# Optimization experiments

Measured on AMD Instinct MI355X. Metric: run time of the kernel, lower is better.

## Reference

```python
import jax, jax.numpy as jnp
import numpy as np

N = 50000       # nodes
E = 1600000     # edges
G = 16          # graphs in batch
NUMCHIP = 16    # node features
NUMEDGE = 8     # edge features
H = 32          # hidden_channels
NEG = 0.2       # LeakyReLU slope (PyG GAT default)


def _wegat_conv(x, ea, src, dst, Wn, bn, We, be, att):
    """Edge-weighted GAT conv: returns (node_out [N,H], edge_out [E,NUMEDGE])."""
    xn = x @ Wn + bn                      # [N, H]
    ea2 = ea @ We + be                    # [E, NUMEDGE]
    xi = xn[dst]                          # [E, H] target features
    xj = xn[src]                          # [E, H] source features
    logits = jnp.concatenate([xi, xj, ea2], axis=-1) @ att   # [E]
    logits = jax.nn.leaky_relu(logits, NEG)
    # numerically stable softmax over incoming edges per destination node
    m = jax.ops.segment_max(logits, dst, num_segments=N)
    m = jnp.where(jnp.isfinite(m), m, 0.0)
    p = jnp.exp(logits - m[dst])
    s = jax.ops.segment_sum(p, dst, num_segments=N)
    alpha = p / (s[dst] + 1e-16)          # [E]
    out = jax.ops.segment_sum(xj * alpha[:, None], dst, num_segments=N)  # [N, H]
    return out, ea2


def setup_inputs() -> dict:
    key = jax.random.key(0)
    ks = jax.random.split(key, 24)

    def gl(k, shape):
        fan_in = shape[0] if len(shape) > 1 else shape[0]
        return jax.random.normal(k, shape, dtype=jnp.float32) * (1.0 / np.sqrt(fan_in))

    inp = {
        'x': jax.random.normal(ks[0], (N, NUMCHIP), dtype=jnp.float32),
        'edge_attr': jax.random.normal(ks[1], (E, NUMEDGE), dtype=jnp.float32),
        'edge_index': jax.random.randint(ks[2], (2, E), 0, N, dtype=jnp.int64),
        'batch': jnp.sort(jax.random.randint(ks[3], (N,), 0, G, dtype=jnp.int64)),
        # layer 1
        'Wn1': gl(ks[4], (NUMCHIP, H)), 'bn1': jnp.zeros((H,), jnp.float32),
        'We1': gl(ks[5], (NUMEDGE, NUMEDGE)), 'be1': jnp.zeros((NUMEDGE,), jnp.float32),
        'att1': gl(ks[6], (2 * H + NUMEDGE,)),
        # layer 2
        'Wn2': gl(ks[7], (H, H)), 'bn2': jnp.zeros((H,), jnp.float32),
        'We2': gl(ks[8], (NUMEDGE, NUMEDGE)), 'be2': jnp.zeros((NUMEDGE,), jnp.float32),
        'att2': gl(ks[9], (2 * H + NUMEDGE,)),
        # layer 3
        'Wn3': gl(ks[10], (H, H)), 'bn3': jnp.zeros((H,), jnp.float32),
        'We3': gl(ks[11], (NUMEDGE, NUMEDGE)), 'be3': jnp.zeros((NUMEDGE,), jnp.float32),
        'att3': gl(ks[12], (2 * H + NUMEDGE,)),
        # head
        'Wlin': gl(ks[13], (H, 1)), 'blin': jnp.zeros((1,), jnp.float32),
    }
    return inp


def reference(x, edge_attr, edge_index, batch,
              Wn1, bn1, We1, be1, att1,
              Wn2, bn2, We2, be2, att2,
              Wn3, bn3, We3, be3, att3,
              Wlin, blin):
    src, dst = edge_index[0], edge_index[1]
    x1, ea1 = _wegat_conv(x, edge_attr, src, dst, Wn1, bn1, We1, be1, att1)
    x1 = jax.nn.relu(x1)  # NOTE: original's edge_attr.relu() is a discarded no-op
    x2, ea2 = _wegat_conv(x1, ea1, src, dst, Wn2, bn2, We2, be2, att2)
    x2 = jax.nn.relu(x2)
    x3, _ = _wegat_conv(x2, ea2, src, dst, Wn3, bn3, We3, be3, att3)
    # global mean pool over graphs
    sums = jax.ops.segment_sum(x3, batch, num_segments=G)                   # [G, H]
    cnts = jax.ops.segment_sum(jnp.ones((N,), x3.dtype), batch, num_segments=G)
    pooled = sums / jnp.maximum(cnts, 1.0)[:, None]
    return pooled @ Wlin + blin  # [G, 1]
```

## Files before the change

### kernel.cpp

```cpp
#include <hip/hip_runtime.h>
#include <math.h>
#include <limits.h>


__global__ __launch_bounds__(256) void hist_kernel(const int* __restrict__ dst, int* cnt, int E) {
    int e = blockIdx.x * blockDim.x + threadIdx.x;
    if (e < E) atomicAdd(&cnt[dst[e]], 1);
}

__global__ __launch_bounds__(1024) void scan_kernel(const int* __restrict__ cnt,
                                                    int* rowptr, int* cursor, int n) {
    __shared__ int sums[1024];
    int t = threadIdx.x;
    int CH = (n + 1023) >> 10;
    int s0 = t * CH;
    int s1 = min(n, s0 + CH);
    int local = 0;
    for (int i = s0; i < s1; i++) local += cnt[i];
    sums[t] = local;
    __syncthreads();
    for (int off = 1; off < 1024; off <<= 1) {
        int v = (t >= off) ? sums[t - off] : 0;
        __syncthreads();
        sums[t] += v;
        __syncthreads();
    }
    int run = (t == 0) ? 0 : sums[t - 1];
    for (int i = s0; i < s1; i++) {
        rowptr[i] = run;
        cursor[i] = run;
        run += cnt[i];
    }
    if (t == 1023) rowptr[n] = sums[1023];
}

__global__ __launch_bounds__(256) void scatter_kernel(const int* __restrict__ src,
                                                      const int* __restrict__ dst,
                                                      int* cursor, int2* __restrict__ pack, int E) {
    int e = blockIdx.x * blockDim.x + threadIdx.x;
    if (e >= E) return;
    int d = dst[e];
    int pos = atomicAdd(&cursor[d], 1);
    pack[pos] = make_int2(src[e], e);
}

template <int IN>
__global__ __launch_bounds__(256) void node_linear(const float* __restrict__ xin,
                                                   const float* __restrict__ Wn,
                                                   const float* __restrict__ bn,
                                                   const float* __restrict__ att,
                                                   float* __restrict__ xn,
                                                   float* __restrict__ ai,
                                                   float* __restrict__ aj, int n) {
    int t = blockIdx.x * blockDim.x + threadIdx.x;
    int node = t >> 5;
    int h = t & 31;
    if (node >= n) return;
    float xv[IN];
    const float4* xr = (const float4*)(xin + (size_t)node * IN);
#pragma unroll
    for (int q = 0; q < IN / 4; q++) {
        float4 f = xr[q];
        xv[4 * q + 0] = f.x;
        xv[4 * q + 1] = f.y;
        xv[4 * q + 2] = f.z;
        xv[4 * q + 3] = f.w;
    }
    float acc = bn[h];
#pragma unroll
    for (int k = 0; k < IN; k++) {
        acc = fmaf(xv[k], Wn[k * 32 + h], acc);
    }
    xn[node * 32 + h] = acc;
    float pi = acc * att[h];
    float pj = acc * att[32 + h];
#pragma unroll
    for (int off = 16; off > 0; off >>= 1) {
        pi += __shfl_xor(pi, off);
        pj += __shfl_xor(pj, off);
    }
    if (h == 0) {
        ai[node] = pi;
        aj[node] = pj;
    }
}

__global__ __launch_bounds__(256) void edge_chain(
    const float* __restrict__ ein,
    const float* __restrict__ We1, const float* __restrict__ be1, const float* __restrict__ a1,
    const float* __restrict__ We2, const float* __restrict__ be2, const float* __restrict__ a2,
    const float* __restrict__ We3, const float* __restrict__ be3, const float* __restrict__ a3,
    float4* __restrict__ aet, int E) {
    int e = blockIdx.x * blockDim.x + threadIdx.x;
    if (e >= E) return;
    const float4* p = (const float4*)(ein + (size_t)e * 8);
    float4 x0 = p[0], x1 = p[1];
    float v[8] = {x0.x, x0.y, x0.z, x0.w, x1.x, x1.y, x1.z, x1.w};
    float t[8], u[8];
    float d1 = 0.f, d2 = 0.f, d3 = 0.f;
#pragma unroll
    for (int j = 0; j < 8; j++) {
        float a = be1[j];
#pragma unroll
        for (int k = 0; k < 8; k++) a = fmaf(v[k], We1[k * 8 + j], a);
        t[j] = a;
        d1 = fmaf(a, a1[j], d1);
    }
#pragma unroll
    for (int j = 0; j < 8; j++) {
        float a = be2[j];
#pragma unroll
        for (int k = 0; k < 8; k++) a = fmaf(t[k], We2[k * 8 + j], a);
        u[j] = a;
        d2 = fmaf(a, a2[j], d2);
    }
#pragma unroll
    for (int j = 0; j < 8; j++) {
        float a = be3[j];
#pragma unroll
        for (int k = 0; k < 8; k++) a = fmaf(u[k], We3[k * 8 + j], a);
        d3 = fmaf(a, a3[j], d3);
    }
    aet[e] = make_float4(d1, d2, d3, 0.f);
}

__global__ __launch_bounds__(256) void row_sort(const int2* __restrict__ pack,
                                                const int* __restrict__ rowptr,
                                                const float4* __restrict__ aet,
                                                int* __restrict__ srcs,
                                                float* __restrict__ aes1,
                                                float* __restrict__ aes2,
                                                float* __restrict__ aes3, int n) {
    int wave = (blockIdx.x * blockDim.x + threadIdx.x) >> 6;
    int lane = threadIdx.x & 63;
    if (wave >= n) return;
    int row = rowptr[wave];
    int deg = rowptr[wave + 1] - row;
    if (deg == 0) return;

    if (deg <= 64) {
        int e = INT_MAX, s = 0;
        if (lane < deg) {
            int2 q = pack[row + lane];
            s = q.x;
            e = q.y;
        }
#pragma unroll
        for (int size = 2; size <= 64; size <<= 1) {
#pragma unroll
            for (int stride = size >> 1; stride > 0; stride >>= 1) {
                int pe = __shfl_xor(e, stride);
                int ps = __shfl_xor(s, stride);
                bool up = ((lane & size) == 0);
                bool lower = ((lane & stride) == 0);
                bool keep = (lower == up) ? (e <= pe) : (e >= pe);
                e = keep ? e : pe;
                s = keep ? s : ps;
            }
        }
        if (lane < deg) {
            srcs[row + lane] = s;
            float4 a = aet[e];
            aes1[row + lane] = a.x;
            aes2[row + lane] = a.y;
            aes3[row + lane] = a.z;
        }
        return;
    }

    int prev = -1;
    for (int r = 0; r < deg; r++) {
        int mn = INT_MAX, ms = 0;
        for (int k = lane; k < deg; k += 64) {
            int2 q = pack[row + k];
            if (q.y > prev && q.y < mn) {
                mn = q.y;
                ms = q.x;
            }
        }
#pragma unroll
        for (int off = 32; off > 0; off >>= 1) {
            int oe = __shfl_xor(mn, off);
            int os = __shfl_xor(ms, off);
            if (oe < mn) {
                mn = oe;
                ms = os;
            }
        }
        if (lane == 0) {
            srcs[row + r] = ms;
            float4 a = aet[mn];
            aes1[row + r] = a.x;
            aes2[row + r] = a.y;
            aes3[row + r] = a.z;
        }
        prev = mn;
    }
}

__global__ __launch_bounds__(256) void gat_aggregate(const float* __restrict__ xn,
                                                     const float* __restrict__ ai,
                                                     const float* __restrict__ aj,
                                                     const float* __restrict__ aes,
                                                     const int* __restrict__ rowptr,
                                                     const int* __restrict__ srcs,
                                                     float* __restrict__ xout,
                                                     int n, int relu_out) {
    int wave = (blockIdx.x * blockDim.x + threadIdx.x) >> 6;
    int lane = threadIdx.x & 63;
    if (wave >= n) return;
    int node = wave;
    int row = rowptr[node];
    int deg = rowptr[node + 1] - row;
    int h = lane & 31;
    if (deg == 0) {
        if (lane < 32) xout[node * 32 + h] = 0.f;
        return;
    }
    float a_i = ai[node];
    const int* sp = srcs + row;
    const float* ap = aes + row;

    if (deg <= 64) {
        int s = 0;
        float lg = -INFINITY;
        bool act = (lane < deg);
        if (act) {
            s = sp[lane];
            lg = a_i + aj[s] + ap[lane];
            lg = (lg >= 0.f) ? lg : 0.2f * lg;
        }
        float mx = lg;
#pragma unroll
        for (int off = 32; off > 0; off >>= 1) mx = fmaxf(mx, __shfl_xor(mx, off));
        float p = act ? expf(lg - mx) : 0.f;
        float ps = 0.f;
        for (int j = 0; j < deg; j++) ps += __shfl(p, j);
        float al = p / (ps + 1e-16f);
        float acc = 0.f;
        int j = 0;
        for (; j + 3 < deg; j += 4) {
            float a0 = __shfl(al, j);
            int s0 = __shfl(s, j);
            float a1 = __shfl(al, j + 1);
            int s1 = __shfl(s, j + 1);
            float a2 = __shfl(al, j + 2);
            int s2 = __shfl(s, j + 2);
            float a3 = __shfl(al, j + 3);
            int s3 = __shfl(s, j + 3);
            float g0 = xn[s0 * 32 + h];
            float g1 = xn[s1 * 32 + h];
            float g2 = xn[s2 * 32 + h];
            float g3 = xn[s3 * 32 + h];
            acc = __fadd_rn(acc, __fmul_rn(a0, g0));
            acc = __fadd_rn(acc, __fmul_rn(a1, g1));
            acc = __fadd_rn(acc, __fmul_rn(a2, g2));
            acc = __fadd_rn(acc, __fmul_rn(a3, g3));
        }
        for (; j < deg; j++) {
            float aj_ = __shfl(al, j);
            int sj = __shfl(s, j);
            acc = __fadd_rn(acc, __fmul_rn(aj_, xn[sj * 32 + h]));
        }
        float o = acc;
        if (relu_out) o = fmaxf(o, 0.f);
        if (lane < 32) xout[node * 32 + h] = o;
        return;
    }

    float mx = -INFINITY;
    for (int k = lane; k < deg; k += 64) {
        float lg = a_i + aj[sp[k]] + ap[k];
        lg = (lg >= 0.f) ? lg : 0.2f * lg;
        mx = fmaxf(mx, lg);
    }
#pragma unroll
    for (int off = 32; off > 0; off >>= 1) mx = fmaxf(mx, __shfl_xor(mx, off));

    float ps = 0.f;
    for (int base = 0; base < deg; base += 64) {
        int k = base + lane;
        float p = 0.f;
        if (k < deg) {
            float lg = a_i + aj[sp[k]] + ap[k];
            lg = (lg >= 0.f) ? lg : 0.2f * lg;
            p = expf(lg - mx);
        }
        int csize = min(64, deg - base);
        for (int j = 0; j < csize; j++) ps += __shfl(p, j);
    }
    float denom = ps + 1e-16f;
    float acc = 0.f;
    for (int base = 0; base < deg; base += 64) {
        int k = base + lane;
        float p = 0.f;
        int s = 0;
        if (k < deg) {
            s = sp[k];
            float lg = a_i + aj[s] + ap[k];
            lg = (lg >= 0.f) ? lg : 0.2f * lg;
            p = expf(lg - mx);
        }
        float al = p / denom;
        int csize = min(64, deg - base);
        for (int j = 0; j < csize; j++) {
            float aj_ = __shfl(al, j);
            int sj = __shfl(s, j);
            acc = __fadd_rn(acc, __fmul_rn(aj_, xn[sj * 32 + h]));
        }
    }
    float o = acc;
    if (relu_out) o = fmaxf(o, 0.f);
    if (lane < 32) xout[node * 32 + h] = o;
}

__global__ __launch_bounds__(1024) void poolhead_kernel(const float* __restrict__ x3,
                                                        const int* __restrict__ batch,
                                                        const float* __restrict__ Wlin,
                                                        const float* __restrict__ blin,
                                                        float* out, int n) {
    __shared__ float red[32][33];
    int g = blockIdx.x;
    int t = threadIdx.x;
    int h = t & 31;
    int rowl = t >> 5;
    int lo = 0, hi = n;
    while (lo < hi) {
        int m = (lo + hi) >> 1;
        if (batch[m] < g) lo = m + 1; else hi = m;
    }
    int start = lo;
    lo = start; hi = n;
    while (lo < hi) {
        int m = (lo + hi) >> 1;
        if (batch[m] < g + 1) lo = m + 1; else hi = m;
    }
    int end = lo;
    float acc = 0.f;
    for (int i = start + rowl; i < end; i += 32) acc += x3[i * 32 + h];
    red[rowl][h] = acc;
    __syncthreads();
    if (rowl < 16) red[rowl][h] = red[rowl][h] + red[rowl + 16][h];
    __syncthreads();
    if (rowl < 8) red[rowl][h] = red[rowl][h] + red[rowl + 8][h];
    __syncthreads();
    if (rowl < 4) red[rowl][h] = red[rowl][h] + red[rowl + 4][h];
    __syncthreads();
    if (rowl < 2) red[rowl][h] = red[rowl][h] + red[rowl + 2][h];
    __syncthreads();
    if (rowl == 0) {
        float s = red[0][h] + red[1][h];
        float c = fmaxf((float)(end - start), 1.f);
        float pooled = s / c;
        float sum = 0.f;
        for (int k = 0; k < 32; k++) {
            float v = __shfl(pooled, k, 32);
            sum = __fadd_rn(sum, __fmul_rn(v, Wlin[k]));
        }
        if (h == 0) out[g] = sum + blin[0];
    }
}

extern "C" void kernel_launch(void* const* d_in, const int* in_sizes, int n_in,
                              void* d_out, int out_size, void* d_ws, size_t ws_size,
                              hipStream_t stream) {
    const float* x    = (const float*)d_in[0];
    const float* ea0  = (const float*)d_in[1];
    const int* ei     = (const int*)d_in[2];
    const int* batch  = (const int*)d_in[3];
    const float* Wn[3] = {(const float*)d_in[4], (const float*)d_in[9],  (const float*)d_in[14]};
    const float* bn[3] = {(const float*)d_in[5], (const float*)d_in[10], (const float*)d_in[15]};
    const float* We[3] = {(const float*)d_in[6], (const float*)d_in[11], (const float*)d_in[16]};
    const float* be[3] = {(const float*)d_in[7], (const float*)d_in[12], (const float*)d_in[17]};
    const float* att[3]= {(const float*)d_in[8], (const float*)d_in[13], (const float*)d_in[18]};
    const float* Wlin = (const float*)d_in[19];
    const float* blin = (const float*)d_in[20];
    float* out = (float*)d_out;

    const int N = in_sizes[0] / 16;
    const int E = in_sizes[1] / 8;
    const int G = out_size;
    (void)n_in; (void)ws_size;

    const int* srcp = ei;
    const int* dstp = ei + E;

    char* base = (char*)d_ws;
    size_t off = 0;
    auto carve = [&](size_t bytes) -> void* {
        void* p = base + off;
        off = (off + bytes + 255) & ~(size_t)255;
        return p;
    };
    float* aes1  = (float*)carve((size_t)E * 4);
    float* aes2  = (float*)carve((size_t)E * 4);
    float* aes3  = (float*)carve((size_t)E * 4);
    int* srcs    = (int*)carve((size_t)E * 4);
    float* ai    = (float*)carve((size_t)N * 4);
    float* aj    = (float*)carve((size_t)N * 4);
    int* cnt     = (int*)carve((size_t)N * 4);
    int* rowptr  = (int*)carve((size_t)(N + 1) * 4);
    int* cursor  = (int*)carve((size_t)N * 4);
    int2* pack   = (int2*)carve((size_t)E * 8);

    char* trans = base + off;
    float4* aet = (float4*)trans;
    float* xnA  = (float*)trans;
    float* xnB  = xnA + (size_t)N * 32;

    int ebks = (E + 255) / 256;
    int nhbks = (N * 32 + 255) / 256;
    int aggbks = (N + 3) / 4;

    hipMemsetAsync(cnt, 0, (size_t)N * 4, stream);
    hist_kernel<<<ebks, 256, 0, stream>>>(dstp, cnt, E);
    scan_kernel<<<1, 1024, 0, stream>>>(cnt, rowptr, cursor, N);
    scatter_kernel<<<ebks, 256, 0, stream>>>(srcp, dstp, cursor, pack, E);

    edge_chain<<<ebks, 256, 0, stream>>>(ea0,
                                         We[0], be[0], att[0] + 64,
                                         We[1], be[1], att[1] + 64,
                                         We[2], be[2], att[2] + 64,
                                         aet, E);

    row_sort<<<aggbks, 256, 0, stream>>>(pack, rowptr, aet,
                                         srcs, aes1, aes2, aes3, N);

    node_linear<16><<<nhbks, 256, 0, stream>>>(x, Wn[0], bn[0], att[0], xnA, ai, aj, N);
    gat_aggregate<<<aggbks, 256, 0, stream>>>(xnA, ai, aj, aes1, rowptr, srcs, xnB, N, 1);

    node_linear<32><<<nhbks, 256, 0, stream>>>(xnB, Wn[1], bn[1], att[1], xnA, ai, aj, N);
    gat_aggregate<<<aggbks, 256, 0, stream>>>(xnA, ai, aj, aes2, rowptr, srcs, xnB, N, 1);

    node_linear<32><<<nhbks, 256, 0, stream>>>(xnB, Wn[2], bn[2], att[2], xnA, ai, aj, N);
    gat_aggregate<<<aggbks, 256, 0, stream>>>(xnA, ai, aj, aes3, rowptr, srcs, xnB, N, 0);

    poolhead_kernel<<<G, 1024, 0, stream>>>(xnB, batch, Wlin, blin, out, N);
}
```

Measured before the change: 753.5 us.

## Fuse edge-attribute chain into row sort and use readlane in aggregation

Removes the separate edge_chain kernel and its float4 intermediate buffer by computing the three per-edge attention terms inside row_sort, directly from the original edge attributes after sorting. This saves one kernel launch plus a write and a random re-read of the aet array. In exchange the edge reads in row_sort become gathers ordered by the sorted edge ids, and the large-degree path computes on lane 0 only. Separately, the small-degree aggregation path replaces variable-trip shuffle loops with fully unrolled 64-iteration readlane loops. That path always does 64 gathers even for low-degree nodes, relying on inactive lanes holding s=0 and al=0.

```diff
diff --git a/kernel.cpp b/kernel.cpp
--- a/kernel.cpp
+++ b/kernel.cpp
@@ -2,6 +2,10 @@
 #include <math.h>
 #include <limits.h>
 
+
+__device__ __forceinline__ float rlane(float v, int j) {
+    return __uint_as_float(__builtin_amdgcn_readlane(__float_as_uint(v), j));
+}
 
 __global__ __launch_bounds__(256) void hist_kernel(const int* __restrict__ dst, int* cnt, int E) {
     int e = blockIdx.x * blockDim.x + threadIdx.x;
@@ -85,14 +89,12 @@
     }
 }
 
-__global__ __launch_bounds__(256) void edge_chain(
-    const float* __restrict__ ein,
+__device__ __forceinline__ void edge_chain_compute(
+    const float* __restrict__ ein, int e,
     const float* __restrict__ We1, const float* __restrict__ be1, const float* __restrict__ a1,
     const float* __restrict__ We2, const float* __restrict__ be2, const float* __restrict__ a2,
     const float* __restrict__ We3, const float* __restrict__ be3, const float* __restrict__ a3,
-    float4* __restrict__ aet, int E) {
-    int e = blockIdx.x * blockDim.x + threadIdx.x;
-    if (e >= E) return;
+    float& d1o, float& d2o, float& d3o) {
     const float4* p = (const float4*)(ein + (size_t)e * 8);
     float4 x0 = p[0], x1 = p[1];
     float v[8] = {x0.x, x0.y, x0.z, x0.w, x1.x, x1.y, x1.z, x1.w};
@@ -121,16 +123,19 @@
         for (int k = 0; k < 8; k++) a = fmaf(u[k], We3[k * 8 + j], a);
         d3 = fmaf(a, a3[j], d3);
     }
-    aet[e] = make_float4(d1, d2, d3, 0.f);
-}
-
-__global__ __launch_bounds__(256) void row_sort(const int2* __restrict__ pack,
-                                                const int* __restrict__ rowptr,
-                                                const float4* __restrict__ aet,
-                                                int* __restrict__ srcs,
-                                                float* __restrict__ aes1,
-                                                float* __restrict__ aes2,
-                                                float* __restrict__ aes3, int n) {
+    d1o = d1;
+    d2o = d2;
+    d3o = d3;
+}
+
+__global__ __launch_bounds__(256) void row_sort(
+    const int2* __restrict__ pack, const int* __restrict__ rowptr,
+    const float* __restrict__ ein,
+    const float* __restrict__ We1, const float* __restrict__ be1, const float* __restrict__ a1,
+    const float* __restrict__ We2, const float* __restrict__ be2, const float* __restrict__ a2,
+    const float* __restrict__ We3, const float* __restrict__ be3, const float* __restrict__ a3,
+    int* __restrict__ srcs,
+    float* __restrict__ aes1, float* __restrict__ aes2, float* __restrict__ aes3, int n) {
     int wave = (blockIdx.x * blockDim.x + threadIdx.x) >> 6;
     int lane = threadIdx.x & 63;
     if (wave >= n) return;
@@ -160,10 +165,11 @@
         }
         if (lane < deg) {
             srcs[row + lane] = s;
-            float4 a = aet[e];
-            aes1[row + lane] = a.x;
-            aes2[row + lane] = a.y;
-            aes3[row + lane] = a.z;
+            float d1, d2, d3;
+            edge_chain_compute(ein, e, We1, be1, a1, We2, be2, a2, We3, be3, a3, d1, d2, d3);
+            aes1[row + lane] = d1;
+            aes2[row + lane] = d2;
+            aes3[row + lane] = d3;
         }
         return;
     }
@@ -189,10 +195,11 @@
         }
         if (lane == 0) {
             srcs[row + r] = ms;
-            float4 a = aet[mn];
-            aes1[row + r] = a.x;
-            aes2[row + r] = a.y;
-            aes3[row + r] = a.z;
+            float d1, d2, d3;
+            edge_chain_compute(ein, mn, We1, be1, a1, We2, be2, a2, We3, be3, a3, d1, d2, d3);
+            aes1[row + r] = d1;
+            aes2[row + r] = d2;
+            aes3[row + r] = d3;
         }
         prev = mn;
     }
@@ -235,32 +242,16 @@
         for (int off = 32; off > 0; off >>= 1) mx = fmaxf(mx, __shfl_xor(mx, off));
         float p = act ? expf(lg - mx) : 0.f;
         float ps = 0.f;
-        for (int j = 0; j < deg; j++) ps += __shfl(p, j);
+#pragma unroll
+        for (int j = 0; j < 64; j++) ps += rlane(p, j);
         float al = p / (ps + 1e-16f);
         float acc = 0.f;
-        int j = 0;
-        for (; j + 3 < deg; j += 4) {
-            float a0 = __shfl(al, j);
-            int s0 = __shfl(s, j);
-            float a1 = __shfl(al, j + 1);
-            int s1 = __shfl(s, j + 1);
-            float a2 = __shfl(al, j + 2);
-            int s2 = __shfl(s, j + 2);
-            float a3 = __shfl(al, j + 3);
-            int s3 = __shfl(s, j + 3);
-            float g0 = xn[s0 * 32 + h];
-            float g1 = xn[s1 * 32 + h];
-            float g2 = xn[s2 * 32 + h];
-            float g3 = xn[s3 * 32 + h];
-            acc = __fadd_rn(acc, __fmul_rn(a0, g0));
-            acc = __fadd_rn(acc, __fmul_rn(a1, g1));
-            acc = __fadd_rn(acc, __fmul_rn(a2, g2));
-            acc = __fadd_rn(acc, __fmul_rn(a3, g3));
-        }
-        for (; j < deg; j++) {
-            float aj_ = __shfl(al, j);
-            int sj = __shfl(s, j);
-            acc = __fadd_rn(acc, __fmul_rn(aj_, xn[sj * 32 + h]));
+#pragma unroll
+        for (int j = 0; j < 64; j++) {
+            int sj = __builtin_amdgcn_readlane(s, j);
+            float alj = rlane(al, j);
+            float g = xn[sj * 32 + h];
+            acc = __fadd_rn(acc, __fmul_rn(alj, g));
         }
         float o = acc;
         if (relu_out) o = fmaxf(o, 0.f);
@@ -402,11 +393,8 @@
     int* rowptr  = (int*)carve((size_t)(N + 1) * 4);
     int* cursor  = (int*)carve((size_t)N * 4);
     int2* pack   = (int2*)carve((size_t)E * 8);
-
-    char* trans = base + off;
-    float4* aet = (float4*)trans;
-    float* xnA  = (float*)trans;
-    float* xnB  = xnA + (size_t)N * 32;
+    float* xnA   = (float*)carve((size_t)N * 32 * 4);
+    float* xnB   = (float*)carve((size_t)N * 32 * 4);
 
     int ebks = (E + 255) / 256;
     int nhbks = (N * 32 + 255) / 256;
@@ -417,13 +405,10 @@
     scan_kernel<<<1, 1024, 0, stream>>>(cnt, rowptr, cursor, N);
     scatter_kernel<<<ebks, 256, 0, stream>>>(srcp, dstp, cursor, pack, E);
 
-    edge_chain<<<ebks, 256, 0, stream>>>(ea0,
+    row_sort<<<aggbks, 256, 0, stream>>>(pack, rowptr, ea0,
                                          We[0], be[0], att[0] + 64,
                                          We[1], be[1], att[1] + 64,
                                          We[2], be[2], att[2] + 64,
-                                         aet, E);
-
-    row_sort<<<aggbks, 256, 0, stream>>>(pack, rowptr, aet,
                                          srcs, aes1, aes2, aes3, N);
 
     node_linear<16><<<nhbks, 256, 0, stream>>>(x, Wn[0], bn[0], att[0], xnA, ai, aj, N);
```

New measurement: 744.3 us. About the same (-1.2%).
